# Kernel tuning notes

Measured on AMD Instinct MI355X. Metric: run time of the kernel, lower is better.

Reference implementation:

```python
import jax, jax.numpy as jnp
import numpy as np

T = 524288          # 2**19 hash table size per level (power of 2)
F = 2               # features per table entry
NL = [16, 22, 30, 42, 58, 80, 111, 153, 212, 293, 406, 561, 775, 1071, 1481, 2046]
L_DIR = 4           # direction positional encoding freqs: 3 + 2*4*3 = 27
AABB = 3.0
PI1, PI2, PI3 = 1, 2654435761, 805459861
N_PTS = 1000000

_BITS = np.array([[(v >> k) & 1 for k in range(3)] for v in range(8)], dtype=bool)  # [8,3] corner offsets


def _linear(key, fan_in, fan_out):
    lim = 1.0 / np.sqrt(fan_in)
    kw, kb = jax.random.split(key)
    W = jax.random.uniform(kw, (fan_in, fan_out), jnp.float32, -lim, lim)
    b = jax.random.uniform(kb, (fan_out,), jnp.float32, -lim, lim)
    return W, b


def setup_inputs() -> dict:
    key = jax.random.key(0)
    ks = jax.random.split(key, 8)
    x = jax.random.normal(ks[0], (N_PTS, 3), jnp.float32)   # world-space sample points
    d = jax.random.normal(ks[1], (N_PTS, 3), jnp.float32)   # view directions
    tables = (jax.random.uniform(ks[2], (len(NL), T, F), jnp.float32) * 2 - 1) * 1e-4
    dW1, db1 = _linear(ks[3], F * len(NL), 64)
    dW2, db2 = _linear(ks[4], 64, 16)
    cW1, cb1 = _linear(ks[5], 27 + 16, 64)
    cW2, cb2 = _linear(ks[6], 64, 64)
    cW3, cb3 = _linear(ks[7], 64, 3)
    return dict(x=x, d=d, tables=tables, dW1=dW1, db1=db1, dW2=dW2, db2=db2,
                cW1=cW1, cb1=cb1, cW2=cW2, cb2=cb2, cW3=cW3, cb3=cb3)


def _hash_encode(xs, tables):
    # xs: [n,3] in [0,1]^3. Multi-resolution hash grid + trilinear interpolation.
    bits = jnp.asarray(_BITS)  # [8,3] bool
    feats = []
    for i, n in enumerate(NL):
        xn = xs * n
        fl = jnp.floor(xn)
        w = xn - fl                                   # [n,3] trilinear weights
        fl_i = fl.astype(jnp.uint32)
        ce_i = jnp.ceil(xn).astype(jnp.uint32)
        corner = jnp.where(bits[None], ce_i[:, None, :], fl_i[:, None, :])   # [n,8,3]
        # spatial hash: xor of coord * prime, mod T; T is 2**19 so uint32
        # wraparound multiply is exact mod T (bit-mask)
        h = ((corner[..., 0] * jnp.uint32(PI1))
             ^ (corner[..., 1] * jnp.uint32(PI2))
             ^ (corner[..., 2] * jnp.uint32(PI3))) & jnp.uint32(T - 1)       # [n,8]
        vals = tables[i][h]                            # [n,8,F] irregular gather
        wc = jnp.prod(jnp.where(bits[None], w[:, None, :], 1.0 - w[:, None, :]), axis=-1)  # [n,8]
        feats.append(jnp.einsum('nv,nvf->nf', wc, vals))
    return jnp.concatenate(feats, axis=1)              # [n, F*len(NL)] = [n,32]


def _pos_enc(d):
    outs = [d]
    for i in range(L_DIR):
        outs.append(jnp.sin((2.0 ** i) * d))
        outs.append(jnp.cos((2.0 ** i) * d))
    return jnp.concatenate(outs, axis=1)               # [n,27]


def reference(x, d, tables, dW1, db1, dW2, db2, cW1, cb1, cW2, cb2, cW3, cb3):
    xs = x / AABB
    mask = (jnp.abs(xs[:, 0]) < 0.5) & (jnp.abs(xs[:, 1]) < 0.5) & (jnp.abs(xs[:, 2]) < 0.5)
    xs = jnp.clip(xs + 0.5, 0.0, 1.0)                  # out-of-box rows get masked below
    feats = _hash_encode(xs, tables)
    h = jnp.maximum(feats @ dW1 + db1, 0.0) @ dW2 + db2            # [n,16] density MLP
    c_in = jnp.concatenate([h, _pos_enc(d)], axis=1)               # [n,43]
    hid = jnp.maximum(c_in @ cW1 + cb1, 0.0)
    hid = jnp.maximum(hid @ cW2 + cb2, 0.0)
    col = jax.nn.sigmoid(hid @ cW3 + cb3)                          # [n,3]
    color = jnp.where(mask[:, None], col, 0.0)
    log_sigma = jnp.where(mask, h[:, 0], -10000.0)
    return color, jnp.exp(log_sigma)
```

## Files before the change

### kernel.cpp

```cpp
#include <hip/hip_runtime.h>
#include <hip/hip_bf16.h>
#include <stdint.h>

#define TS 524288u
#define TMASK (TS - 1u)
#define QTOTAL 331757
#define NHL 11

typedef __attribute__((ext_vector_type(8))) short bf16x8;
typedef __attribute__((ext_vector_type(4))) float f32x4;

__device__ __forceinline__ short f2bf(float f) {
    union { float f; uint32_t u; } v; v.f = f;
    const uint32_t r = (v.u + 0x7fffu + ((v.u >> 16) & 1u)) >> 16;
    return (short)r;
}
__device__ __forceinline__ uint32_t cvtpk(float a, float b) {
    uint32_t r;
    asm("v_cvt_pk_bf16_f32 %0, %1, %2" : "=v"(r) : "v"(a), "v"(b));
    return r;
}
__device__ __forceinline__ short bf1(float a) { return (short)(cvtpk(a, a) & 0xffffu); }
__device__ __forceinline__ float bflo(uint32_t u) { return __uint_as_float(u << 16); }
__device__ __forceinline__ float bfhi(uint32_t u) { return __uint_as_float(u & 0xffff0000u); }
__device__ __forceinline__ uint32_t pack2(float a, float b) {
    return (uint32_t)(uint16_t)f2bf(a) | ((uint32_t)(uint16_t)f2bf(b) << 16);
}

__constant__ float c_NLf[16] = {16.f,22.f,30.f,42.f,58.f,80.f,111.f,153.f,
                                212.f,293.f,406.f,561.f,775.f,1071.f,1481.f,2046.f};
__constant__ int c_NP1[5]  = {17, 23, 31, 43, 59};
__constant__ int c_QOFF[5] = {0, 4913, 17080, 46871, 126378};

__global__ __launch_bounds__(256)
void cvt_tables_h(const float2* __restrict__ src, uint32_t* __restrict__ dst, int npairs)
{
    const int i = blockIdx.x * 256 + threadIdx.x;
    if (i >= npairs) return;
    const float2 v = src[i];
    dst[i] = pack2(v.x, v.y);
}

__global__ __launch_bounds__(256)
void build_quad(const float2* __restrict__ tbf, uint4* __restrict__ quad)
{
    const int i = blockIdx.x * 256 + threadIdx.x;
    if (i >= QTOTAL) return;
    int l, base;
    if      (i <   4913) { l = 0; base = 0;      }
    else if (i <  17080) { l = 1; base = 4913;   }
    else if (i <  46871) { l = 2; base = 17080;  }
    else if (i < 126378) { l = 3; base = 46871;  }
    else                 { l = 4; base = 126378; }
    const int np1 = c_NP1[l];
    int r = i - base;
    const int z = r % np1; r /= np1;
    const int y = r % np1;
    const int x = r / np1;
    const float2* tb = tbf + (size_t)l * TS;
    const uint32_t hx  = (uint32_t)x;
    const uint32_t hy0 = (uint32_t)y       * 2654435761u;
    const uint32_t hy1 = (uint32_t)(y + 1) * 2654435761u;
    const uint32_t hz0 = (uint32_t)z       * 805459861u;
    const uint32_t hz1 = (uint32_t)(z + 1) * 805459861u;
    const float2 a = tb[(hx ^ hy0 ^ hz0) & TMASK];
    const float2 b = tb[(hx ^ hy0 ^ hz1) & TMASK];
    const float2 c = tb[(hx ^ hy1 ^ hz0) & TMASK];
    const float2 d = tb[(hx ^ hy1 ^ hz1) & TMASK];
    uint4 q;
    q.x = pack2(a.x, a.y);
    q.y = pack2(b.x, b.y);
    q.z = pack2(c.x, c.y);
    q.w = pack2(d.x, d.y);
    quad[i] = q;
}

__device__ __forceinline__ uint32_t enc_pt(const int l, const float sx, const float sy,
                                           const float sz,
                                           const uint32_t* __restrict__ tb16h,
                                           const uint4* __restrict__ qtab)
{
    const float nf = c_NLf[l];
    const float xn0 = sx * nf, xn1 = sy * nf, xn2 = sz * nf;
    const float fl0 = floorf(xn0), fl1 = floorf(xn1), fl2 = floorf(xn2);
    const float w0 = xn0 - fl0, w1 = xn1 - fl1, w2 = xn2 - fl2;
    const uint32_t f0 = (uint32_t)fl0, f1 = (uint32_t)fl1, f2 = (uint32_t)fl2;

    float v0x,v0y,v1x,v1y,v2x,v2y,v3x,v3y,v4x,v4y,v5x,v5y,v6x,v6y,v7x,v7y;

    if (l < 5) {
        const int np1 = c_NP1[l];
        const uint4* qt = qtab + c_QOFF[l];
        const int cell = ((int)f0 * np1 + (int)f1) * np1 + (int)f2;
        const uint4 qa = qt[cell];
        const uint4 qb = qt[cell + np1 * np1];
        v0x = bflo(qa.x); v0y = bfhi(qa.x);
        v4x = bflo(qa.y); v4y = bfhi(qa.y);
        v2x = bflo(qa.z); v2y = bfhi(qa.z);
        v6x = bflo(qa.w); v6y = bfhi(qa.w);
        v1x = bflo(qb.x); v1y = bfhi(qb.x);
        v5x = bflo(qb.y); v5y = bfhi(qb.y);
        v3x = bflo(qb.z); v3y = bfhi(qb.z);
        v7x = bflo(qb.w); v7y = bfhi(qb.w);
    } else {
        const uint32_t c0 = (uint32_t)ceilf(xn0);
        const uint32_t c1 = (uint32_t)ceilf(xn1);
        const uint32_t c2 = (uint32_t)ceilf(xn2);
        const uint32_t hyf = f1 * 2654435761u, hyc = c1 * 2654435761u;
        const uint32_t hzf = f2 * 805459861u,  hzc = c2 * 805459861u;
        const uint32_t* tb = tb16h + (size_t)(l - 5) * TS;
        const uint32_t Sff = hyf ^ hzf, Scf = hyc ^ hzf;
        const uint32_t Sfc = hyf ^ hzc, Scc = hyc ^ hzc;
        uint32_t e0,e1,e2,e3,e4,e5,e6,e7;
        if ((f0 ^ c0) == 1u) {
            const uint32_t h0 = (f0 ^ Sff) & TMASK;
            const uint32_t h2 = (f0 ^ Scf) & TMASK;
            const uint32_t h4 = (f0 ^ Sfc) & TMASK;
            const uint32_t h6 = (f0 ^ Scc) & TMASK;
            const uint2 t0 = *reinterpret_cast<const uint2*>(tb + (h0 & ~1u));
            const uint2 t2 = *reinterpret_cast<const uint2*>(tb + (h2 & ~1u));
            const uint2 t4 = *reinterpret_cast<const uint2*>(tb + (h4 & ~1u));
            const uint2 t6 = *reinterpret_cast<const uint2*>(tb + (h6 & ~1u));
            e0 = (h0 & 1u) ? t0.y : t0.x;  e1 = (h0 & 1u) ? t0.x : t0.y;
            e2 = (h2 & 1u) ? t2.y : t2.x;  e3 = (h2 & 1u) ? t2.x : t2.y;
            e4 = (h4 & 1u) ? t4.y : t4.x;  e5 = (h4 & 1u) ? t4.x : t4.y;
            e6 = (h6 & 1u) ? t6.y : t6.x;  e7 = (h6 & 1u) ? t6.x : t6.y;
        } else {
            e0 = tb[(f0 ^ Sff) & TMASK];  e1 = tb[(c0 ^ Sff) & TMASK];
            e2 = tb[(f0 ^ Scf) & TMASK];  e3 = tb[(c0 ^ Scf) & TMASK];
            e4 = tb[(f0 ^ Sfc) & TMASK];  e5 = tb[(c0 ^ Sfc) & TMASK];
            e6 = tb[(f0 ^ Scc) & TMASK];  e7 = tb[(c0 ^ Scc) & TMASK];
        }
        v0x = bflo(e0); v0y = bfhi(e0); v1x = bflo(e1); v1y = bfhi(e1);
        v2x = bflo(e2); v2y = bfhi(e2); v3x = bflo(e3); v3y = bfhi(e3);
        v4x = bflo(e4); v4y = bfhi(e4); v5x = bflo(e5); v5y = bfhi(e5);
        v6x = bflo(e6); v6y = bfhi(e6); v7x = bflo(e7); v7y = bfhi(e7);
    }

    const float u0 = 1.0f - w0, u1 = 1.0f - w1, u2 = 1.0f - w2;
    float a0, a1;
    a0 = u0*u1*u2 * v0x;              a1 = u0*u1*u2 * v0y;
    a0 = fmaf(w0*u1*u2, v1x, a0);     a1 = fmaf(w0*u1*u2, v1y, a1);
    a0 = fmaf(u0*w1*u2, v2x, a0);     a1 = fmaf(u0*w1*u2, v2y, a1);
    a0 = fmaf(w0*w1*u2, v3x, a0);     a1 = fmaf(w0*w1*u2, v3y, a1);
    a0 = fmaf(u0*u1*w2, v4x, a0);     a1 = fmaf(u0*u1*w2, v4y, a1);
    a0 = fmaf(w0*u1*w2, v5x, a0);     a1 = fmaf(w0*u1*w2, v5y, a1);
    a0 = fmaf(u0*w1*w2, v6x, a0);     a1 = fmaf(u0*w1*w2, v6y, a1);
    a0 = fmaf(w0*w1*w2, v7x, a0);     a1 = fmaf(w0*w1*w2, v7y, a1);

    return cvtpk(a0, a1);
}

__global__ __launch_bounds__(256)
void ngp_encode_lm(const float* __restrict__ xg, const uint32_t* __restrict__ tb16h,
                   const uint4* __restrict__ qtab, uint32_t* __restrict__ feats_lm,
                   const int n, const unsigned tiles)
{
    const unsigned b = blockIdx.x;
    const int l = (int)(b / tiles);
    const int p = (int)(b - (unsigned)l * tiles) * 256 + threadIdx.x;
    if (p >= n) return;

    float sx = xg[3*p+0] / 3.0f, sy = xg[3*p+1] / 3.0f, sz = xg[3*p+2] / 3.0f;
    if (!((fabsf(sx) < 0.5f) && (fabsf(sy) < 0.5f) && (fabsf(sz) < 0.5f))) {
        feats_lm[(size_t)l * n + p] = 0u;
        return;
    }
    sx = fminf(fmaxf(sx + 0.5f, 0.0f), 1.0f);
    sy = fminf(fmaxf(sy + 0.5f, 0.0f), 1.0f);
    sz = fminf(fmaxf(sz + 0.5f, 0.0f), 1.0f);
    feats_lm[(size_t)l * n + p] = enc_pt(l, sx, sy, sz, tb16h, qtab);
}

__global__ __launch_bounds__(256)
void ngp_encode_f32(const float* __restrict__ xg, const float2* __restrict__ tbf,
                    uint32_t* __restrict__ feats_lm, const int n, const unsigned tiles)
{
    const unsigned b = blockIdx.x;
    const int l = (int)(b / tiles);
    const int p = (int)(b - (unsigned)l * tiles) * 256 + threadIdx.x;
    if (p >= n) return;
    float sx = xg[3*p+0] / 3.0f, sy = xg[3*p+1] / 3.0f, sz = xg[3*p+2] / 3.0f;
    if (!((fabsf(sx) < 0.5f) && (fabsf(sy) < 0.5f) && (fabsf(sz) < 0.5f))) {
        feats_lm[(size_t)l * n + p] = 0u;
        return;
    }
    sx = fminf(fmaxf(sx + 0.5f, 0.0f), 1.0f);
    sy = fminf(fmaxf(sy + 0.5f, 0.0f), 1.0f);
    sz = fminf(fmaxf(sz + 0.5f, 0.0f), 1.0f);
    const float nf = c_NLf[l];
    const float xn0 = sx*nf, xn1 = sy*nf, xn2 = sz*nf;
    const float fl0 = floorf(xn0), fl1 = floorf(xn1), fl2 = floorf(xn2);
    const float w0 = xn0-fl0, w1 = xn1-fl1, w2 = xn2-fl2;
    const uint32_t f0=(uint32_t)fl0, f1=(uint32_t)fl1, f2=(uint32_t)fl2;
    const uint32_t c0=(uint32_t)ceilf(xn0), c1=(uint32_t)ceilf(xn1), c2=(uint32_t)ceilf(xn2);
    const uint32_t hyf = f1*2654435761u, hyc = c1*2654435761u;
    const uint32_t hzf = f2*805459861u,  hzc = c2*805459861u;
    const float2* tb = tbf + (size_t)l * TS;
    const float2 e0 = tb[(f0^hyf^hzf)&TMASK], e1 = tb[(c0^hyf^hzf)&TMASK];
    const float2 e2 = tb[(f0^hyc^hzf)&TMASK], e3 = tb[(c0^hyc^hzf)&TMASK];
    const float2 e4 = tb[(f0^hyf^hzc)&TMASK], e5 = tb[(c0^hyf^hzc)&TMASK];
    const float2 e6 = tb[(f0^hyc^hzc)&TMASK], e7 = tb[(c0^hyc^hzc)&TMASK];
    const float u0 = 1.0f-w0, u1 = 1.0f-w1, u2 = 1.0f-w2;
    float a0, a1;
    a0 = u0*u1*u2 * e0.x;             a1 = u0*u1*u2 * e0.y;
    a0 = fmaf(w0*u1*u2, e1.x, a0);    a1 = fmaf(w0*u1*u2, e1.y, a1);
    a0 = fmaf(u0*w1*u2, e2.x, a0);    a1 = fmaf(u0*w1*u2, e2.y, a1);
    a0 = fmaf(w0*w1*u2, e3.x, a0);    a1 = fmaf(w0*w1*u2, e3.y, a1);
    a0 = fmaf(u0*u1*w2, e4.x, a0);    a1 = fmaf(u0*u1*w2, e4.y, a1);
    a0 = fmaf(w0*u1*w2, e5.x, a0);    a1 = fmaf(w0*u1*w2, e5.y, a1);
    a0 = fmaf(u0*w1*w2, e6.x, a0);    a1 = fmaf(u0*w1*w2, e6.y, a1);
    a0 = fmaf(w0*w1*w2, e7.x, a0);    a1 = fmaf(w0*w1*w2, e7.y, a1);
    feats_lm[(size_t)l * n + p] = pack2(a0, a1);
}

#define ACT_STRIDE 72

__global__ __launch_bounds__(256, 2)
void ngp_mlp_mfma(const float* __restrict__ xg, const float* __restrict__ dg,
                  const uint32_t* __restrict__ feats_lm,
                  const float* __restrict__ dW1, const float* __restrict__ db1,
                  const float* __restrict__ dW2, const float* __restrict__ db2,
                  const float* __restrict__ cW1, const float* __restrict__ cb1,
                  const float* __restrict__ cW2, const float* __restrict__ cb2,
                  const float* __restrict__ cW3, const float* __restrict__ cb3,
                  float* __restrict__ out, int n)
{
    __shared__ __align__(16) short w1[2048];
    __shared__ __align__(16) short w2[1024];
    __shared__ __align__(16) short w3[4096];
    __shared__ __align__(16) short w4[4096];
    __shared__ __align__(16) short w5[1024];
    __shared__ __align__(16) float b1[64];
    __shared__ __align__(16) float b2[16];
    __shared__ __align__(16) float b3[64];
    __shared__ __align__(16) float b4[64];
    __shared__ __align__(16) float b5[16];
    __shared__ __align__(16) short act[4][16*ACT_STRIDE];

    const int tid = threadIdx.x;

    for (int i2 = tid; i2 < 4*16*ACT_STRIDE/2; i2 += 256)
        reinterpret_cast<uint32_t*>(act)[i2] = 0u;

    for (int i2 = tid; i2 < 2048; i2 += 256) {
        const int jb = i2 >> 9, lane = (i2 >> 3) & 63, e = i2 & 7;
        const int j = jb*16 + (lane & 15), k = ((lane >> 4) << 3) + e;
        w1[i2] = f2bf(dW1[k*64 + j]);
    }
    for (int i2 = tid; i2 < 1024; i2 += 256) {
        const int kb = i2 >> 9, lane = (i2 >> 3) & 63, e = i2 & 7;
        const int j = lane & 15, k = kb*32 + ((lane >> 4) << 3) + e;
        w2[i2] = f2bf(dW2[k*16 + j]);
    }
    for (int i2 = tid; i2 < 4096; i2 += 256) {
        const int jb = i2 >> 10, kb = (i2 >> 9) & 1, lane = (i2 >> 3) & 63, e = i2 & 7;
        const int j = jb*16 + (lane & 15), k = kb*32 + ((lane >> 4) << 3) + e;
        w3[i2] = (k < 43) ? f2bf(cW1[k*64 + j]) : (short)0;
        w4[i2] = f2bf(cW2[k*64 + j]);
    }
    for (int i2 = tid; i2 < 1024; i2 += 256) {
        const int kb = i2 >> 9, lane = (i2 >> 3) & 63, e = i2 & 7;
        const int j = lane & 15, k = kb*32 + ((lane >> 4) << 3) + e;
        w5[i2] = (j < 3) ? f2bf(cW3[k*3 + j]) : (short)0;
    }
    if (tid < 64) { b1[tid] = db1[tid]; b3[tid] = cb1[tid]; b4[tid] = cb2[tid]; }
    if (tid < 16) { b2[tid] = db2[tid]; b5[tid] = (tid < 3) ? cb3[tid] : 0.0f; }
    __syncthreads();

    const int wv = tid >> 6, lane = tid & 63;
    const int p16 = lane & 15, quad = lane >> 4;
    const int dc = (quad < 3) ? quad : 0;
    short* buf = &act[wv][0];

    bf16x8 A1[4], A2[2], A3[8], A4[8], A5[2];
    #pragma unroll
    for (int jb = 0; jb < 4; ++jb) A1[jb] = *reinterpret_cast<const bf16x8*>(&w1[(jb*64 + lane)*8]);
    #pragma unroll
    for (int kb = 0; kb < 2; ++kb) A2[kb] = *reinterpret_cast<const bf16x8*>(&w2[(kb*64 + lane)*8]);
    #pragma unroll
    for (int i = 0; i < 8; ++i) {
        A3[i] = *reinterpret_cast<const bf16x8*>(&w3[(i*64 + lane)*8]);
        A4[i] = *reinterpret_cast<const bf16x8*>(&w4[(i*64 + lane)*8]);
    }
    #pragma unroll
    for (int kb = 0; kb < 2; ++kb) A5[kb] = *reinterpret_cast<const bf16x8*>(&w5[(kb*64 + lane)*8]);
    f32x4 B1[4], B3[4], B4[4];
    #pragma unroll
    for (int jb = 0; jb < 4; ++jb) {
        B1[jb] = *reinterpret_cast<const f32x4*>(&b1[jb*16 + quad*4]);
        B3[jb] = *reinterpret_cast<const f32x4*>(&b3[jb*16 + quad*4]);
        B4[jb] = *reinterpret_cast<const f32x4*>(&b4[jb*16 + quad*4]);
    }
    const f32x4 B2v = *reinterpret_cast<const f32x4*>(&b2[quad*4]);
    const f32x4 B5v = *reinterpret_cast<const f32x4*>(&b5[quad*4]);

    const int ntiles = (n + 63) >> 6;
    int t = blockIdx.x;
    if (t >= ntiles) return;

    int pp_n; bool valid_n;
    uint32_t fn0, fn1, fn2, fn3;
    float xn0, xn1, xn2, dn;

    auto issue = [&](int tt) {
        const int pr = tt*64 + wv*16 + p16;
        valid_n = (pr < n);
        pp_n = valid_n ? pr : (n - 1);
        fn0 = feats_lm[(size_t)(4*quad+0)*n + pp_n];
        fn1 = feats_lm[(size_t)(4*quad+1)*n + pp_n];
        fn2 = feats_lm[(size_t)(4*quad+2)*n + pp_n];
        fn3 = feats_lm[(size_t)(4*quad+3)*n + pp_n];
        xn0 = xg[3*pp_n+0];
        xn1 = xg[3*pp_n+1];
        xn2 = xg[3*pp_n+2];
        dn  = dg[3*pp_n + dc];
    };

    issue(t);
    while (t < ntiles) {
        const int pp = pp_n;
        const bool valid = valid_n;
        const uint32_t fc0 = fn0, fc1 = fn1, fc2 = fn2, fc3 = fn3;
        const float xc0 = xn0, xc1 = xn1, xc2 = xn2;
        const float dv = dn;

        const int t2 = t + gridDim.x;
        if (t2 < ntiles) issue(t2);

        const bool inside = (fabsf(xc0 / 3.0f) < 0.5f) && (fabsf(xc1 / 3.0f) < 0.5f)
                         && (fabsf(xc2 / 3.0f) < 0.5f);

        union { int4 i; bf16x8 v; } bu;
        bu.i.x = (int)fc0; bu.i.y = (int)fc1; bu.i.z = (int)fc2; bu.i.w = (int)fc3;
        const bf16x8 bA = bu.v;
        #pragma unroll
        for (int jb = 0; jb < 4; ++jb) {
            const int j0 = jb*16 + quad*4;
            f32x4 acc = B1[jb];
            acc = __builtin_amdgcn_mfma_f32_16x16x32_bf16(A1[jb], bA, acc, 0, 0, 0);
            uint2 s;
            s.x = cvtpk(fmaxf(acc[0], 0.f), fmaxf(acc[1], 0.f));
            s.y = cvtpk(fmaxf(acc[2], 0.f), fmaxf(acc[3], 0.f));
            *reinterpret_cast<uint2*>(&buf[p16*ACT_STRIDE + j0]) = s;
        }

        {
            const bf16x8 bF0 = *reinterpret_cast<const bf16x8*>(&buf[p16*ACT_STRIDE + quad*8]);
            const bf16x8 bF1 = *reinterpret_cast<const bf16x8*>(&buf[p16*ACT_STRIDE + 32 + quad*8]);
            f32x4 acc2 = B2v;
            acc2 = __builtin_amdgcn_mfma_f32_16x16x32_bf16(A2[0], bF0, acc2, 0, 0, 0);
            acc2 = __builtin_amdgcn_mfma_f32_16x16x32_bf16(A2[1], bF1, acc2, 0, 0, 0);
            if (quad == 0 && valid)
                out[(size_t)3*n + pp] = inside ? __expf(acc2[0]) : 0.0f;
            uint2 s;
            s.x = cvtpk(acc2[0], acc2[1]);
            s.y = cvtpk(acc2[2], acc2[3]);
            *reinterpret_cast<uint2*>(&buf[p16*ACT_STRIDE + quad*4]) = s;
        }
        if (quad < 3) {
            buf[p16*ACT_STRIDE + 16 + quad] = bf1(dv);
            float arg = dv;
            #pragma unroll
            for (int f = 0; f < 4; ++f) {
                buf[p16*ACT_STRIDE + 19 + 6*f + quad] = bf1(__sinf(arg));
                buf[p16*ACT_STRIDE + 22 + 6*f + quad] = bf1(__cosf(arg));
                arg += arg;
            }
        }

        {
            const bf16x8 bF0 = *reinterpret_cast<const bf16x8*>(&buf[p16*ACT_STRIDE + quad*8]);
            const bf16x8 bF1 = *reinterpret_cast<const bf16x8*>(&buf[p16*ACT_STRIDE + 32 + quad*8]);
            #pragma unroll
            for (int jb = 0; jb < 4; ++jb) {
                const int j0 = jb*16 + quad*4;
                f32x4 acc = B3[jb];
                acc = __builtin_amdgcn_mfma_f32_16x16x32_bf16(A3[jb*2 + 0], bF0, acc, 0, 0, 0);
                acc = __builtin_amdgcn_mfma_f32_16x16x32_bf16(A3[jb*2 + 1], bF1, acc, 0, 0, 0);
                uint2 s;
                s.x = cvtpk(fmaxf(acc[0], 0.f), fmaxf(acc[1], 0.f));
                s.y = cvtpk(fmaxf(acc[2], 0.f), fmaxf(acc[3], 0.f));
                *reinterpret_cast<uint2*>(&buf[p16*ACT_STRIDE + j0]) = s;
            }
        }

        {
            const bf16x8 bF0 = *reinterpret_cast<const bf16x8*>(&buf[p16*ACT_STRIDE + quad*8]);
            const bf16x8 bF1 = *reinterpret_cast<const bf16x8*>(&buf[p16*ACT_STRIDE + 32 + quad*8]);
            #pragma unroll
            for (int jb = 0; jb < 4; ++jb) {
                const int j0 = jb*16 + quad*4;
                f32x4 acc = B4[jb];
                acc = __builtin_amdgcn_mfma_f32_16x16x32_bf16(A4[jb*2 + 0], bF0, acc, 0, 0, 0);
                acc = __builtin_amdgcn_mfma_f32_16x16x32_bf16(A4[jb*2 + 1], bF1, acc, 0, 0, 0);
                uint2 s;
                s.x = cvtpk(fmaxf(acc[0], 0.f), fmaxf(acc[1], 0.f));
                s.y = cvtpk(fmaxf(acc[2], 0.f), fmaxf(acc[3], 0.f));
                *reinterpret_cast<uint2*>(&buf[p16*ACT_STRIDE + j0]) = s;
            }
        }

        {
            const bf16x8 bF0 = *reinterpret_cast<const bf16x8*>(&buf[p16*ACT_STRIDE + quad*8]);
            const bf16x8 bF1 = *reinterpret_cast<const bf16x8*>(&buf[p16*ACT_STRIDE + 32 + quad*8]);
            f32x4 acc5 = B5v;
            acc5 = __builtin_amdgcn_mfma_f32_16x16x32_bf16(A5[0], bF0, acc5, 0, 0, 0);
            acc5 = __builtin_amdgcn_mfma_f32_16x16x32_bf16(A5[1], bF1, acc5, 0, 0, 0);
            if (quad == 0 && valid) {
                #pragma unroll
                for (int r = 0; r < 3; ++r) {
                    const float s = 1.0f / (1.0f + __expf(-acc5[r]));
                    out[3*(size_t)pp + r] = inside ? s : 0.0f;
                }
            }
        }
        t = t2;
    }
}

extern "C" void kernel_launch(void* const* d_in, const int* in_sizes, int n_in,
                              void* d_out, int out_size, void* d_ws, size_t ws_size,
                              hipStream_t stream)
{
    const float* x   = (const float*)d_in[0];
    const float* d   = (const float*)d_in[1];
    const float* tb  = (const float*)d_in[2];
    const float* dW1 = (const float*)d_in[3];
    const float* db1 = (const float*)d_in[4];
    const float* dW2 = (const float*)d_in[5];
    const float* db2 = (const float*)d_in[6];
    const float* cW1 = (const float*)d_in[7];
    const float* cb1 = (const float*)d_in[8];
    const float* cW2 = (const float*)d_in[9];
    const float* cb2 = (const float*)d_in[10];
    const float* cW3 = (const float*)d_in[11];
    const float* cb3 = (const float*)d_in[12];
    float* out = (float*)d_out;

    const int n = in_sizes[0] / 3;

    size_t off = 0;
    uint32_t* feats_lm = (uint32_t*)d_ws;                 off += (size_t)n * 16 * 4;
    uint32_t* tb16h    = (uint32_t*)((char*)d_ws + off);  off += (size_t)NHL * TS * 4;
    uint4*    quadbuf  = (uint4*)((char*)d_ws + off);     off += (size_t)QTOTAL * 16;
    const bool planA = (ws_size >= off);

    const unsigned tiles = (unsigned)((n + 255) / 256);

    if (planA) {
        {
            const int npairs = NHL * (int)TS;
            hipLaunchKernelGGL(cvt_tables_h, dim3((npairs + 255) / 256), dim3(256), 0, stream,
                               (const float2*)tb + 5 * (size_t)TS, tb16h, npairs);
        }
        hipLaunchKernelGGL(build_quad, dim3((QTOTAL + 255) / 256), dim3(256), 0, stream,
                           (const float2*)tb, quadbuf);
        hipLaunchKernelGGL(ngp_encode_lm, dim3(tiles * 16), dim3(256), 0, stream,
                           x, tb16h, quadbuf, feats_lm, n, tiles);
    } else {
        hipLaunchKernelGGL(ngp_encode_f32, dim3(tiles * 16), dim3(256), 0, stream,
                           x, (const float2*)tb, feats_lm, n, tiles);
    }
    {
        const int ntiles = (n + 63) >> 6;
        const int nblk = (ntiles < 512) ? ntiles : 512;
        dim3 block(256), grid(nblk);
        hipLaunchKernelGGL(ngp_mlp_mfma, grid, block, 0, stream,
                           x, d, feats_lm, dW1, db1, dW2, db2,
                           cW1, cb1, cW2, cb2, cW3, cb3, out, n);
    }
}
```

Before: 367.5 us.

## Precompute normalized points once and raise MLP occupancy with bias reloads

Adds a prep kernel that normalizes and clips the sample points once, marking out-of-box points with a sentinel, so the 16 per-level encode blocks and the MLP no longer repeat the divide and box test. The MLP kernel stops holding biases in registers and reads them from shared memory, moves launch bounds from 2 to 3 waves per SIMD, widens the grid cap from 512 to 768 blocks, and pads the activation stride from 72 to 76. The cost is an extra kernel launch plus a 12-byte-per-point buffer write and read, and the encode kernel still reads three floats per point.

```diff
diff --git a/kernel.cpp b/kernel.cpp
--- a/kernel.cpp
+++ b/kernel.cpp
@@ -73,6 +73,26 @@
     q.z = pack2(c.x, c.y);
     q.w = pack2(d.x, d.y);
     quad[i] = q;
+}
+
+__global__ __launch_bounds__(256)
+void prep_pts(const float* __restrict__ xg, float* __restrict__ prep, int n)
+{
+    const int i = blockIdx.x * 256 + threadIdx.x;
+    if (i >= n) return;
+    const float sx = xg[3*i+0] / 3.0f;
+    const float sy = xg[3*i+1] / 3.0f;
+    const float sz = xg[3*i+2] / 3.0f;
+    const bool inside = (fabsf(sx) < 0.5f) && (fabsf(sy) < 0.5f) && (fabsf(sz) < 0.5f);
+    if (inside) {
+        prep[3*i+0] = fminf(fmaxf(sx + 0.5f, 0.0f), 1.0f);
+        prep[3*i+1] = fminf(fmaxf(sy + 0.5f, 0.0f), 1.0f);
+        prep[3*i+2] = fminf(fmaxf(sz + 0.5f, 0.0f), 1.0f);
+    } else {
+        prep[3*i+0] = -1.0f;
+        prep[3*i+1] = 0.0f;
+        prep[3*i+2] = 0.0f;
+    }
 }
 
 __device__ __forceinline__ uint32_t enc_pt(const int l, const float sx, const float sy,
@@ -151,8 +171,9 @@
     return cvtpk(a0, a1);
 }
 
+template<bool HASPREP>
 __global__ __launch_bounds__(256)
-void ngp_encode_lm(const float* __restrict__ xg, const uint32_t* __restrict__ tb16h,
+void ngp_encode_lm(const float* __restrict__ xp, const uint32_t* __restrict__ tb16h,
                    const uint4* __restrict__ qtab, uint32_t* __restrict__ feats_lm,
                    const int n, const unsigned tiles)
 {
@@ -161,15 +182,21 @@
     const int p = (int)(b - (unsigned)l * tiles) * 256 + threadIdx.x;
     if (p >= n) return;
 
-    float sx = xg[3*p+0] / 3.0f, sy = xg[3*p+1] / 3.0f, sz = xg[3*p+2] / 3.0f;
-    if (!((fabsf(sx) < 0.5f) && (fabsf(sy) < 0.5f) && (fabsf(sz) < 0.5f))) {
-        feats_lm[(size_t)l * n + p] = 0u;
-        return;
-    }
-    sx = fminf(fmaxf(sx + 0.5f, 0.0f), 1.0f);
-    sy = fminf(fmaxf(sy + 0.5f, 0.0f), 1.0f);
-    sz = fminf(fmaxf(sz + 0.5f, 0.0f), 1.0f);
-    feats_lm[(size_t)l * n + p] = enc_pt(l, sx, sy, sz, tb16h, qtab);
+    if (HASPREP) {
+        const float s0 = xp[3*p+0], s1 = xp[3*p+1], s2 = xp[3*p+2];
+        if (s0 < 0.0f) { feats_lm[(size_t)l * n + p] = 0u; return; }
+        feats_lm[(size_t)l * n + p] = enc_pt(l, s0, s1, s2, tb16h, qtab);
+    } else {
+        float sx = xp[3*p+0] / 3.0f, sy = xp[3*p+1] / 3.0f, sz = xp[3*p+2] / 3.0f;
+        if (!((fabsf(sx) < 0.5f) && (fabsf(sy) < 0.5f) && (fabsf(sz) < 0.5f))) {
+            feats_lm[(size_t)l * n + p] = 0u;
+            return;
+        }
+        sx = fminf(fmaxf(sx + 0.5f, 0.0f), 1.0f);
+        sy = fminf(fmaxf(sy + 0.5f, 0.0f), 1.0f);
+        sz = fminf(fmaxf(sz + 0.5f, 0.0f), 1.0f);
+        feats_lm[(size_t)l * n + p] = enc_pt(l, sx, sy, sz, tb16h, qtab);
+    }
 }
 
 __global__ __launch_bounds__(256)
@@ -214,10 +241,11 @@
     feats_lm[(size_t)l * n + p] = pack2(a0, a1);
 }
 
-#define ACT_STRIDE 72
-
-__global__ __launch_bounds__(256, 2)
-void ngp_mlp_mfma(const float* __restrict__ xg, const float* __restrict__ dg,
+#define ACT_STRIDE 76
+
+template<bool HASPREP>
+__global__ __launch_bounds__(256, 3)
+void ngp_mlp_mfma(const float* __restrict__ xp, const float* __restrict__ dg,
                   const uint32_t* __restrict__ feats_lm,
                   const float* __restrict__ dW1, const float* __restrict__ db1,
                   const float* __restrict__ dW2, const float* __restrict__ db2,
@@ -285,15 +313,6 @@
     }
     #pragma unroll
     for (int kb = 0; kb < 2; ++kb) A5[kb] = *reinterpret_cast<const bf16x8*>(&w5[(kb*64 + lane)*8]);
-    f32x4 B1[4], B3[4], B4[4];
-    #pragma unroll
-    for (int jb = 0; jb < 4; ++jb) {
-        B1[jb] = *reinterpret_cast<const f32x4*>(&b1[jb*16 + quad*4]);
-        B3[jb] = *reinterpret_cast<const f32x4*>(&b3[jb*16 + quad*4]);
-        B4[jb] = *reinterpret_cast<const f32x4*>(&b4[jb*16 + quad*4]);
-    }
-    const f32x4 B2v = *reinterpret_cast<const f32x4*>(&b2[quad*4]);
-    const f32x4 B5v = *reinterpret_cast<const f32x4*>(&b5[quad*4]);
 
     const int ntiles = (n + 63) >> 6;
     int t = blockIdx.x;
@@ -301,7 +320,7 @@
 
     int pp_n; bool valid_n;
     uint32_t fn0, fn1, fn2, fn3;
-    float xn0, xn1, xn2, dn;
+    float in0, in1, in2, dn;
 
     auto issue = [&](int tt) {
         const int pr = tt*64 + wv*16 + p16;
@@ -311,9 +330,13 @@
         fn1 = feats_lm[(size_t)(4*quad+1)*n + pp_n];
         fn2 = feats_lm[(size_t)(4*quad+2)*n + pp_n];
         fn3 = feats_lm[(size_t)(4*quad+3)*n + pp_n];
-        xn0 = xg[3*pp_n+0];
-        xn1 = xg[3*pp_n+1];
-        xn2 = xg[3*pp_n+2];
+        if (HASPREP) {
+            in0 = xp[3*pp_n];
+        } else {
+            in0 = xp[3*pp_n+0];
+            in1 = xp[3*pp_n+1];
+            in2 = xp[3*pp_n+2];
+        }
         dn  = dg[3*pp_n + dc];
     };
 
@@ -322,14 +345,19 @@
         const int pp = pp_n;
         const bool valid = valid_n;
         const uint32_t fc0 = fn0, fc1 = fn1, fc2 = fn2, fc3 = fn3;
-        const float xc0 = xn0, xc1 = xn1, xc2 = xn2;
+        const float ic0 = in0, ic1 = in1, ic2 = in2;
         const float dv = dn;
 
         const int t2 = t + gridDim.x;
         if (t2 < ntiles) issue(t2);
 
-        const bool inside = (fabsf(xc0 / 3.0f) < 0.5f) && (fabsf(xc1 / 3.0f) < 0.5f)
-                         && (fabsf(xc2 / 3.0f) < 0.5f);
+        bool inside;
+        if (HASPREP) {
+            inside = (ic0 >= 0.0f);
+        } else {
+            inside = (fabsf(ic0 / 3.0f) < 0.5f) && (fabsf(ic1 / 3.0f) < 0.5f)
+                  && (fabsf(ic2 / 3.0f) < 0.5f);
+        }
 
         union { int4 i; bf16x8 v; } bu;
         bu.i.x = (int)fc0; bu.i.y = (int)fc1; bu.i.z = (int)fc2; bu.i.w = (int)fc3;
@@ -337,7 +365,7 @@
         #pragma unroll
         for (int jb = 0; jb < 4; ++jb) {
             const int j0 = jb*16 + quad*4;
-            f32x4 acc = B1[jb];
+            f32x4 acc = *reinterpret_cast<const f32x4*>(&b1[j0]);
             acc = __builtin_amdgcn_mfma_f32_16x16x32_bf16(A1[jb], bA, acc, 0, 0, 0);
             uint2 s;
             s.x = cvtpk(fmaxf(acc[0], 0.f), fmaxf(acc[1], 0.f));
@@ -348,7 +376,7 @@
         {
             const bf16x8 bF0 = *reinterpret_cast<const bf16x8*>(&buf[p16*ACT_STRIDE + quad*8]);
             const bf16x8 bF1 = *reinterpret_cast<const bf16x8*>(&buf[p16*ACT_STRIDE + 32 + quad*8]);
-            f32x4 acc2 = B2v;
+            f32x4 acc2 = *reinterpret_cast<const f32x4*>(&b2[quad*4]);
             acc2 = __builtin_amdgcn_mfma_f32_16x16x32_bf16(A2[0], bF0, acc2, 0, 0, 0);
             acc2 = __builtin_amdgcn_mfma_f32_16x16x32_bf16(A2[1], bF1, acc2, 0, 0, 0);
             if (quad == 0 && valid)
@@ -375,7 +403,7 @@
             #pragma unroll
             for (int jb = 0; jb < 4; ++jb) {
                 const int j0 = jb*16 + quad*4;
-                f32x4 acc = B3[jb];
+                f32x4 acc = *reinterpret_cast<const f32x4*>(&b3[j0]);
                 acc = __builtin_amdgcn_mfma_f32_16x16x32_bf16(A3[jb*2 + 0], bF0, acc, 0, 0, 0);
                 acc = __builtin_amdgcn_mfma_f32_16x16x32_bf16(A3[jb*2 + 1], bF1, acc, 0, 0, 0);
                 uint2 s;
@@ -391,7 +419,7 @@
             #pragma unroll
             for (int jb = 0; jb < 4; ++jb) {
                 const int j0 = jb*16 + quad*4;
-                f32x4 acc = B4[jb];
+                f32x4 acc = *reinterpret_cast<const f32x4*>(&b4[j0]);
                 acc = __builtin_amdgcn_mfma_f32_16x16x32_bf16(A4[jb*2 + 0], bF0, acc, 0, 0, 0);
                 acc = __builtin_amdgcn_mfma_f32_16x16x32_bf16(A4[jb*2 + 1], bF1, acc, 0, 0, 0);
                 uint2 s;
@@ -404,7 +432,7 @@
         {
             const bf16x8 bF0 = *reinterpret_cast<const bf16x8*>(&buf[p16*ACT_STRIDE + quad*8]);
             const bf16x8 bF1 = *reinterpret_cast<const bf16x8*>(&buf[p16*ACT_STRIDE + 32 + quad*8]);
-            f32x4 acc5 = B5v;
+            f32x4 acc5 = *reinterpret_cast<const f32x4*>(&b5[quad*4]);
             acc5 = __builtin_amdgcn_mfma_f32_16x16x32_bf16(A5[0], bF0, acc5, 0, 0, 0);
             acc5 = __builtin_amdgcn_mfma_f32_16x16x32_bf16(A5[1], bF1, acc5, 0, 0, 0);
             if (quad == 0 && valid) {
@@ -444,9 +472,15 @@
     uint32_t* feats_lm = (uint32_t*)d_ws;                 off += (size_t)n * 16 * 4;
     uint32_t* tb16h    = (uint32_t*)((char*)d_ws + off);  off += (size_t)NHL * TS * 4;
     uint4*    quadbuf  = (uint4*)((char*)d_ws + off);     off += (size_t)QTOTAL * 16;
-    const bool planA = (ws_size >= off);
+    const size_t off1 = off;
+    float*    prepbuf  = (float*)((char*)d_ws + off);     off += (size_t)n * 3 * 4;
+    const size_t off2 = off;
+    const bool planA  = (ws_size >= off1);
+    const bool planA2 = (ws_size >= off2);
 
     const unsigned tiles = (unsigned)((n + 255) / 256);
+    const int ntiles = (n + 63) >> 6;
+    const int nblk = (ntiles < 768) ? ntiles : 768;
 
     if (planA) {
         {
@@ -456,17 +490,25 @@
         }
         hipLaunchKernelGGL(build_quad, dim3((QTOTAL + 255) / 256), dim3(256), 0, stream,
                            (const float2*)tb, quadbuf);
-        hipLaunchKernelGGL(ngp_encode_lm, dim3(tiles * 16), dim3(256), 0, stream,
-                           x, tb16h, quadbuf, feats_lm, n, tiles);
+        if (planA2) {
+            hipLaunchKernelGGL(prep_pts, dim3((n + 255) / 256), dim3(256), 0, stream,
+                               x, prepbuf, n);
+            hipLaunchKernelGGL((ngp_encode_lm<true>), dim3(tiles * 16), dim3(256), 0, stream,
+                               prepbuf, tb16h, quadbuf, feats_lm, n, tiles);
+            hipLaunchKernelGGL((ngp_mlp_mfma<true>), dim3(nblk), dim3(256), 0, stream,
+                               prepbuf, d, feats_lm, dW1, db1, dW2, db2,
+                               cW1, cb1, cW2, cb2, cW3, cb3, out, n);
+        } else {
+            hipLaunchKernelGGL((ngp_encode_lm<false>), dim3(tiles * 16), dim3(256), 0, stream,
+                               x, tb16h, quadbuf, feats_lm, n, tiles);
+            hipLaunchKernelGGL((ngp_mlp_mfma<false>), dim3(nblk), dim3(256), 0, stream,
+                               x, d, feats_lm, dW1, db1, dW2, db2,
+                               cW1, cb1, cW2, cb2, cW3, cb3, out, n);
+        }
     } else {
         hipLaunchKernelGGL(ngp_encode_f32, dim3(tiles * 16), dim3(256), 0, stream,
                            x, (const float2*)tb, feats_lm, n, tiles);
-    }
-    {
-        const int ntiles = (n + 63) >> 6;
-        const int nblk = (ntiles < 512) ? ntiles : 512;
-        dim3 block(256), grid(nblk);
-        hipLaunchKernelGGL(ngp_mlp_mfma, grid, block, 0, stream,
+        hipLaunchKernelGGL((ngp_mlp_mfma<false>), dim3(nblk), dim3(256), 0, stream,
                            x, d, feats_lm, dW1, db1, dW2, db2,
                            cW1, cb1, cW2, cb2, cW3, cb3, out, n);
     }
```

Result: slower. 406.8 us (+10.7%).

## Process two 16-point tiles per wave in MLP kernel and use nontemporal feature stores

Applied to the files above, without the earlier changes.

The MLP kernel now interleaves two independent 16-point sub-tiles per wave (A and B), each with its own LDS activation buffer, so back-to-back MFMAs on independent data can hide MFMA and LDS latency. Biases are now read from LDS at each use instead of being held in registers, which frees VGPRs for the doubled state. The encode kernel writes features with nontemporal stores, so these streaming writes are less likely to evict hash-table lines from cache. Risks are higher register pressure and doubled LDS use per block, which could lower occupancy, and fewer persistent tiles per block.

```diff
diff --git a/kernel.cpp b/kernel.cpp
--- a/kernel.cpp
+++ b/kernel.cpp
@@ -163,13 +163,14 @@
 
     float sx = xg[3*p+0] / 3.0f, sy = xg[3*p+1] / 3.0f, sz = xg[3*p+2] / 3.0f;
     if (!((fabsf(sx) < 0.5f) && (fabsf(sy) < 0.5f) && (fabsf(sz) < 0.5f))) {
-        feats_lm[(size_t)l * n + p] = 0u;
+        __builtin_nontemporal_store(0u, &feats_lm[(size_t)l * n + p]);
         return;
     }
     sx = fminf(fmaxf(sx + 0.5f, 0.0f), 1.0f);
     sy = fminf(fmaxf(sy + 0.5f, 0.0f), 1.0f);
     sz = fminf(fmaxf(sz + 0.5f, 0.0f), 1.0f);
-    feats_lm[(size_t)l * n + p] = enc_pt(l, sx, sy, sz, tb16h, qtab);
+    const uint32_t fv = enc_pt(l, sx, sy, sz, tb16h, qtab);
+    __builtin_nontemporal_store(fv, &feats_lm[(size_t)l * n + p]);
 }
 
 __global__ __launch_bounds__(256)
@@ -236,11 +237,11 @@
     __shared__ __align__(16) float b3[64];
     __shared__ __align__(16) float b4[64];
     __shared__ __align__(16) float b5[16];
-    __shared__ __align__(16) short act[4][16*ACT_STRIDE];
+    __shared__ __align__(16) short act[4][32*ACT_STRIDE];
 
     const int tid = threadIdx.x;
 
-    for (int i2 = tid; i2 < 4*16*ACT_STRIDE/2; i2 += 256)
+    for (int i2 = tid; i2 < 4*32*ACT_STRIDE/2; i2 += 256)
         reinterpret_cast<uint32_t*>(act)[i2] = 0u;
 
     for (int i2 = tid; i2 < 2048; i2 += 256) {
@@ -271,7 +272,8 @@
     const int wv = tid >> 6, lane = tid & 63;
     const int p16 = lane & 15, quad = lane >> 4;
     const int dc = (quad < 3) ? quad : 0;
-    short* buf = &act[wv][0];
+    short* bufA = &act[wv][0];
+    short* bufB = &act[wv][16*ACT_STRIDE];
 
     bf16x8 A1[4], A2[2], A3[8], A4[8], A5[2];
     #pragma unroll
@@ -285,133 +287,169 @@
     }
     #pragma unroll
     for (int kb = 0; kb < 2; ++kb) A5[kb] = *reinterpret_cast<const bf16x8*>(&w5[(kb*64 + lane)*8]);
-    f32x4 B1[4], B3[4], B4[4];
-    #pragma unroll
-    for (int jb = 0; jb < 4; ++jb) {
-        B1[jb] = *reinterpret_cast<const f32x4*>(&b1[jb*16 + quad*4]);
-        B3[jb] = *reinterpret_cast<const f32x4*>(&b3[jb*16 + quad*4]);
-        B4[jb] = *reinterpret_cast<const f32x4*>(&b4[jb*16 + quad*4]);
-    }
-    const f32x4 B2v = *reinterpret_cast<const f32x4*>(&b2[quad*4]);
-    const f32x4 B5v = *reinterpret_cast<const f32x4*>(&b5[quad*4]);
-
-    const int ntiles = (n + 63) >> 6;
+
+    const int ntiles = (n + 127) >> 7;
     int t = blockIdx.x;
     if (t >= ntiles) return;
 
-    int pp_n; bool valid_n;
-    uint32_t fn0, fn1, fn2, fn3;
-    float xn0, xn1, xn2, dn;
+    int ppA_n, ppB_n; bool vA_n, vB_n;
+    uint32_t fA0,fA1,fA2,fA3, fB0,fB1,fB2,fB3;
+    float xA0,xA1,xA2, xB0,xB1,xB2, dA_n, dB_n;
 
     auto issue = [&](int tt) {
-        const int pr = tt*64 + wv*16 + p16;
-        valid_n = (pr < n);
-        pp_n = valid_n ? pr : (n - 1);
-        fn0 = feats_lm[(size_t)(4*quad+0)*n + pp_n];
-        fn1 = feats_lm[(size_t)(4*quad+1)*n + pp_n];
-        fn2 = feats_lm[(size_t)(4*quad+2)*n + pp_n];
-        fn3 = feats_lm[(size_t)(4*quad+3)*n + pp_n];
-        xn0 = xg[3*pp_n+0];
-        xn1 = xg[3*pp_n+1];
-        xn2 = xg[3*pp_n+2];
-        dn  = dg[3*pp_n + dc];
+        const int prA = tt*128 + wv*16 + p16;
+        const int prB = prA + 64;
+        vA_n = (prA < n);  ppA_n = vA_n ? prA : (n - 1);
+        vB_n = (prB < n);  ppB_n = vB_n ? prB : (n - 1);
+        fA0 = feats_lm[(size_t)(4*quad+0)*n + ppA_n];
+        fA1 = feats_lm[(size_t)(4*quad+1)*n + ppA_n];
+        fA2 = feats_lm[(size_t)(4*quad+2)*n + ppA_n];
+        fA3 = feats_lm[(size_t)(4*quad+3)*n + ppA_n];
+        fB0 = feats_lm[(size_t)(4*quad+0)*n + ppB_n];
+        fB1 = feats_lm[(size_t)(4*quad+1)*n + ppB_n];
+        fB2 = feats_lm[(size_t)(4*quad+2)*n + ppB_n];
+        fB3 = feats_lm[(size_t)(4*quad+3)*n + ppB_n];
+        xA0 = xg[3*ppA_n+0]; xA1 = xg[3*ppA_n+1]; xA2 = xg[3*ppA_n+2];
+        xB0 = xg[3*ppB_n+0]; xB1 = xg[3*ppB_n+1]; xB2 = xg[3*ppB_n+2];
+        dA_n = dg[3*ppA_n + dc];
+        dB_n = dg[3*ppB_n + dc];
     };
 
     issue(t);
     while (t < ntiles) {
-        const int pp = pp_n;
-        const bool valid = valid_n;
-        const uint32_t fc0 = fn0, fc1 = fn1, fc2 = fn2, fc3 = fn3;
-        const float xc0 = xn0, xc1 = xn1, xc2 = xn2;
-        const float dv = dn;
+        const int ppA = ppA_n, ppB = ppB_n;
+        const bool vA = vA_n, vB = vB_n;
+        const uint32_t a0 = fA0, a1 = fA1, a2 = fA2, a3 = fA3;
+        const uint32_t b0 = fB0, b1v = fB1, b2v = fB2, b3v = fB3;
+        const float cA0 = xA0, cA1 = xA1, cA2 = xA2;
+        const float cB0 = xB0, cB1 = xB1, cB2 = xB2;
+        const float dvA = dA_n, dvB = dB_n;
 
         const int t2 = t + gridDim.x;
         if (t2 < ntiles) issue(t2);
 
-        const bool inside = (fabsf(xc0 / 3.0f) < 0.5f) && (fabsf(xc1 / 3.0f) < 0.5f)
-                         && (fabsf(xc2 / 3.0f) < 0.5f);
-
-        union { int4 i; bf16x8 v; } bu;
-        bu.i.x = (int)fc0; bu.i.y = (int)fc1; bu.i.z = (int)fc2; bu.i.w = (int)fc3;
-        const bf16x8 bA = bu.v;
+        const bool inA = (fabsf(cA0/3.0f) < 0.5f) && (fabsf(cA1/3.0f) < 0.5f) && (fabsf(cA2/3.0f) < 0.5f);
+        const bool inB = (fabsf(cB0/3.0f) < 0.5f) && (fabsf(cB1/3.0f) < 0.5f) && (fabsf(cB2/3.0f) < 0.5f);
+
+        union { int4 i; bf16x8 v; } buA, buB;
+        buA.i.x = (int)a0; buA.i.y = (int)a1; buA.i.z = (int)a2; buA.i.w = (int)a3;
+        buB.i.x = (int)b0; buB.i.y = (int)b1v; buB.i.z = (int)b2v; buB.i.w = (int)b3v;
+        const bf16x8 bAa = buA.v, bAb = buB.v;
         #pragma unroll
         for (int jb = 0; jb < 4; ++jb) {
             const int j0 = jb*16 + quad*4;
-            f32x4 acc = B1[jb];
-            acc = __builtin_amdgcn_mfma_f32_16x16x32_bf16(A1[jb], bA, acc, 0, 0, 0);
-            uint2 s;
-            s.x = cvtpk(fmaxf(acc[0], 0.f), fmaxf(acc[1], 0.f));
-            s.y = cvtpk(fmaxf(acc[2], 0.f), fmaxf(acc[3], 0.f));
-            *reinterpret_cast<uint2*>(&buf[p16*ACT_STRIDE + j0]) = s;
+            const f32x4 bias = *reinterpret_cast<const f32x4*>(&b1[j0]);
+            f32x4 accA = __builtin_amdgcn_mfma_f32_16x16x32_bf16(A1[jb], bAa, bias, 0, 0, 0);
+            f32x4 accB = __builtin_amdgcn_mfma_f32_16x16x32_bf16(A1[jb], bAb, bias, 0, 0, 0);
+            uint2 sA, sB;
+            sA.x = cvtpk(fmaxf(accA[0],0.f), fmaxf(accA[1],0.f));
+            sA.y = cvtpk(fmaxf(accA[2],0.f), fmaxf(accA[3],0.f));
+            sB.x = cvtpk(fmaxf(accB[0],0.f), fmaxf(accB[1],0.f));
+            sB.y = cvtpk(fmaxf(accB[2],0.f), fmaxf(accB[3],0.f));
+            *reinterpret_cast<uint2*>(&bufA[p16*ACT_STRIDE + j0]) = sA;
+            *reinterpret_cast<uint2*>(&bufB[p16*ACT_STRIDE + j0]) = sB;
         }
 
         {
-            const bf16x8 bF0 = *reinterpret_cast<const bf16x8*>(&buf[p16*ACT_STRIDE + quad*8]);
-            const bf16x8 bF1 = *reinterpret_cast<const bf16x8*>(&buf[p16*ACT_STRIDE + 32 + quad*8]);
-            f32x4 acc2 = B2v;
-            acc2 = __builtin_amdgcn_mfma_f32_16x16x32_bf16(A2[0], bF0, acc2, 0, 0, 0);
-            acc2 = __builtin_amdgcn_mfma_f32_16x16x32_bf16(A2[1], bF1, acc2, 0, 0, 0);
-            if (quad == 0 && valid)
-                out[(size_t)3*n + pp] = inside ? __expf(acc2[0]) : 0.0f;
-            uint2 s;
-            s.x = cvtpk(acc2[0], acc2[1]);
-            s.y = cvtpk(acc2[2], acc2[3]);
-            *reinterpret_cast<uint2*>(&buf[p16*ACT_STRIDE + quad*4]) = s;
+            const bf16x8 fA0v = *reinterpret_cast<const bf16x8*>(&bufA[p16*ACT_STRIDE + quad*8]);
+            const bf16x8 fA1v = *reinterpret_cast<const bf16x8*>(&bufA[p16*ACT_STRIDE + 32 + quad*8]);
+            const bf16x8 fB0v = *reinterpret_cast<const bf16x8*>(&bufB[p16*ACT_STRIDE + quad*8]);
+            const bf16x8 fB1v = *reinterpret_cast<const bf16x8*>(&bufB[p16*ACT_STRIDE + 32 + quad*8]);
+            const f32x4 bias = *reinterpret_cast<const f32x4*>(&b2[quad*4]);
+            f32x4 accA = __builtin_amdgcn_mfma_f32_16x16x32_bf16(A2[0], fA0v, bias, 0, 0, 0);
+            f32x4 accB = __builtin_amdgcn_mfma_f32_16x16x32_bf16(A2[0], fB0v, bias, 0, 0, 0);
+            accA = __builtin_amdgcn_mfma_f32_16x16x32_bf16(A2[1], fA1v, accA, 0, 0, 0);
+            accB = __builtin_amdgcn_mfma_f32_16x16x32_bf16(A2[1], fB1v, accB, 0, 0, 0);
+            if (quad == 0 && vA) out[(size_t)3*n + ppA] = inA ? __expf(accA[0]) : 0.0f;
+            if (quad == 0 && vB) out[(size_t)3*n + ppB] = inB ? __expf(accB[0]) : 0.0f;
+            uint2 sA, sB;
+            sA.x = cvtpk(accA[0], accA[1]); sA.y = cvtpk(accA[2], accA[3]);
+            sB.x = cvtpk(accB[0], accB[1]); sB.y = cvtpk(accB[2], accB[3]);
+            *reinterpret_cast<uint2*>(&bufA[p16*ACT_STRIDE + quad*4]) = sA;
+            *reinterpret_cast<uint2*>(&bufB[p16*ACT_STRIDE + quad*4]) = sB;
         }
         if (quad < 3) {
-            buf[p16*ACT_STRIDE + 16 + quad] = bf1(dv);
-            float arg = dv;
+            bufA[p16*ACT_STRIDE + 16 + quad] = bf1(dvA);
+            bufB[p16*ACT_STRIDE + 16 + quad] = bf1(dvB);
+            float argA = dvA, argB = dvB;
             #pragma unroll
             for (int f = 0; f < 4; ++f) {
-                buf[p16*ACT_STRIDE + 19 + 6*f + quad] = bf1(__sinf(arg));
-                buf[p16*ACT_STRIDE + 22 + 6*f + quad] = bf1(__cosf(arg));
-                arg += arg;
+                bufA[p16*ACT_STRIDE + 19 + 6*f + quad] = bf1(__sinf(argA));
+                bufA[p16*ACT_STRIDE + 22 + 6*f + quad] = bf1(__cosf(argA));
+                bufB[p16*ACT_STRIDE + 19 + 6*f + quad] = bf1(__sinf(argB));
+                bufB[p16*ACT_STRIDE + 22 + 6*f + quad] = bf1(__cosf(argB));
+                argA += argA; argB += argB;
             }
         }
 
         {
-            const bf16x8 bF0 = *reinterpret_cast<const bf16x8*>(&buf[p16*ACT_STRIDE + quad*8]);
-            const bf16x8 bF1 = *reinterpret_cast<const bf16x8*>(&buf[p16*ACT_STRIDE + 32 + quad*8]);
+            const bf16x8 fA0v = *reinterpret_cast<const bf16x8*>(&bufA[p16*ACT_STRIDE + quad*8]);
+            const bf16x8 fA1v = *reinterpret_cast<const bf16x8*>(&bufA[p16*ACT_STRIDE + 32 + quad*8]);
+            const bf16x8 fB0v = *reinterpret_cast<const bf16x8*>(&bufB[p16*ACT_STRIDE + quad*8]);
+            const bf16x8 fB1v = *reinterpret_cast<const bf16x8*>(&bufB[p16*ACT_STRIDE + 32 + quad*8]);
             #pragma unroll
             for (int jb = 0; jb < 4; ++jb) {
                 const int j0 = jb*16 + quad*4;
-                f32x4 acc = B3[jb];
-                acc = __builtin_amdgcn_mfma_f32_16x16x32_bf16(A3[jb*2 + 0], bF0, acc, 0, 0, 0);
-                acc = __builtin_amdgcn_mfma_f32_16x16x32_bf16(A3[jb*2 + 1], bF1, acc, 0, 0, 0);
-                uint2 s;
-                s.x = cvtpk(fmaxf(acc[0], 0.f), fmaxf(acc[1], 0.f));
-                s.y = cvtpk(fmaxf(acc[2], 0.f), fmaxf(acc[3], 0.f));
-                *reinterpret_cast<uint2*>(&buf[p16*ACT_STRIDE + j0]) = s;
+                const f32x4 bias = *reinterpret_cast<const f32x4*>(&b3[j0]);
+                f32x4 accA = __builtin_amdgcn_mfma_f32_16x16x32_bf16(A3[jb*2+0], fA0v, bias, 0, 0, 0);
+                f32x4 accB = __builtin_amdgcn_mfma_f32_16x16x32_bf16(A3[jb*2+0], fB0v, bias, 0, 0, 0);
+                accA = __builtin_amdgcn_mfma_f32_16x16x32_bf16(A3[jb*2+1], fA1v, accA, 0, 0, 0);
+                accB = __builtin_amdgcn_mfma_f32_16x16x32_bf16(A3[jb*2+1], fB1v, accB, 0, 0, 0);
+                uint2 sA, sB;
+                sA.x = cvtpk(fmaxf(accA[0],0.f), fmaxf(accA[1],0.f));
+                sA.y = cvtpk(fmaxf(accA[2],0.f), fmaxf(accA[3],0.f));
+                sB.x = cvtpk(fmaxf(accB[0],0.f), fmaxf(accB[1],0.f));
+                sB.y = cvtpk(fmaxf(accB[2],0.f), fmaxf(accB[3],0.f));
+                *reinterpret_cast<uint2*>(&bufA[p16*ACT_STRIDE + j0]) = sA;
+                *reinterpret_cast<uint2*>(&bufB[p16*ACT_STRIDE + j0]) = sB;
             }
         }
 
         {
-            const bf16x8 bF0 = *reinterpret_cast<const bf16x8*>(&buf[p16*ACT_STRIDE + quad*8]);
-            const bf16x8 bF1 = *reinterpret_cast<const bf16x8*>(&buf[p16*ACT_STRIDE + 32 + quad*8]);
+            const bf16x8 fA0v = *reinterpret_cast<const bf16x8*>(&bufA[p16*ACT_STRIDE + quad*8]);
+            const bf16x8 fA1v = *reinterpret_cast<const bf16x8*>(&bufA[p16*ACT_STRIDE + 32 + quad*8]);
+            const bf16x8 fB0v = *reinterpret_cast<const bf16x8*>(&bufB[p16*ACT_STRIDE + quad*8]);
+            const bf16x8 fB1v = *reinterpret_cast<const bf16x8*>(&bufB[p16*ACT_STRIDE + 32 + quad*8]);
             #pragma unroll
             for (int jb = 0; jb < 4; ++jb) {
                 const int j0 = jb*16 + quad*4;
-                f32x4 acc = B4[jb];
-                acc = __builtin_amdgcn_mfma_f32_16x16x32_bf16(A4[jb*2 + 0], bF0, acc, 0, 0, 0);
-                acc = __builtin_amdgcn_mfma_f32_16x16x32_bf16(A4[jb*2 + 1], bF1, acc, 0, 0, 0);
-                uint2 s;
-                s.x = cvtpk(fmaxf(acc[0], 0.f), fmaxf(acc[1], 0.f));
-                s.y = cvtpk(fmaxf(acc[2], 0.f), fmaxf(acc[3], 0.f));
-                *reinterpret_cast<uint2*>(&buf[p16*ACT_STRIDE + j0]) = s;
+                const f32x4 bias = *reinterpret_cast<const f32x4*>(&b4[j0]);
+                f32x4 accA = __builtin_amdgcn_mfma_f32_16x16x32_bf16(A4[jb*2+0], fA0v, bias, 0, 0, 0);
+                f32x4 accB = __builtin_amdgcn_mfma_f32_16x16x32_bf16(A4[jb*2+0], fB0v, bias, 0, 0, 0);
+                accA = __builtin_amdgcn_mfma_f32_16x16x32_bf16(A4[jb*2+1], fA1v, accA, 0, 0, 0);
+                accB = __builtin_amdgcn_mfma_f32_16x16x32_bf16(A4[jb*2+1], fB1v, accB, 0, 0, 0);
+                uint2 sA, sB;
+                sA.x = cvtpk(fmaxf(accA[0],0.f), fmaxf(accA[1],0.f));
+                sA.y = cvtpk(fmaxf(accA[2],0.f), fmaxf(accA[3],0.f));
+                sB.x = cvtpk(fmaxf(accB[0],0.f), fmaxf(accB[1],0.f));
+                sB.y = cvtpk(fmaxf(accB[2],0.f), fmaxf(accB[3],0.f));
+                *reinterpret_cast<uint2*>(&bufA[p16*ACT_STRIDE + j0]) = sA;
+                *reinterpret_cast<uint2*>(&bufB[p16*ACT_STRIDE + j0]) = sB;
             }
         }
 
         {
-            const bf16x8 bF0 = *reinterpret_cast<const bf16x8*>(&buf[p16*ACT_STRIDE + quad*8]);
-            const bf16x8 bF1 = *reinterpret_cast<const bf16x8*>(&buf[p16*ACT_STRIDE + 32 + quad*8]);
-            f32x4 acc5 = B5v;
-            acc5 = __builtin_amdgcn_mfma_f32_16x16x32_bf16(A5[0], bF0, acc5, 0, 0, 0);
-            acc5 = __builtin_amdgcn_mfma_f32_16x16x32_bf16(A5[1], bF1, acc5, 0, 0, 0);
-            if (quad == 0 && valid) {
+            const bf16x8 fA0v = *reinterpret_cast<const bf16x8*>(&bufA[p16*ACT_STRIDE + quad*8]);
+            const bf16x8 fA1v = *reinterpret_cast<const bf16x8*>(&bufA[p16*ACT_STRIDE + 32 + quad*8]);
+            const bf16x8 fB0v = *reinterpret_cast<const bf16x8*>(&bufB[p16*ACT_STRIDE + quad*8]);
+            const bf16x8 fB1v = *reinterpret_cast<const bf16x8*>(&bufB[p16*ACT_STRIDE + 32 + quad*8]);
+            const f32x4 bias = *reinterpret_cast<const f32x4*>(&b5[quad*4]);
+            f32x4 accA = __builtin_amdgcn_mfma_f32_16x16x32_bf16(A5[0], fA0v, bias, 0, 0, 0);
+            f32x4 accB = __builtin_amdgcn_mfma_f32_16x16x32_bf16(A5[0], fB0v, bias, 0, 0, 0);
+            accA = __builtin_amdgcn_mfma_f32_16x16x32_bf16(A5[1], fA1v, accA, 0, 0, 0);
+            accB = __builtin_amdgcn_mfma_f32_16x16x32_bf16(A5[1], fB1v, accB, 0, 0, 0);
+            if (quad == 0 && vA) {
                 #pragma unroll
                 for (int r = 0; r < 3; ++r) {
-                    const float s = 1.0f / (1.0f + __expf(-acc5[r]));
-                    out[3*(size_t)pp + r] = inside ? s : 0.0f;
+                    const float s = 1.0f / (1.0f + __expf(-accA[r]));
+                    out[3*(size_t)ppA + r] = inA ? s : 0.0f;
+                }
+            }
+            if (quad == 0 && vB) {
+                #pragma unroll
+                for (int r = 0; r < 3; ++r) {
+                    const float s = 1.0f / (1.0f + __expf(-accB[r]));
+                    out[3*(size_t)ppB + r] = inB ? s : 0.0f;
                 }
             }
         }
@@ -447,6 +485,8 @@
     const bool planA = (ws_size >= off);
 
     const unsigned tiles = (unsigned)((n + 255) / 256);
+    const int ntiles = (n + 127) >> 7;
+    const int nblk = (ntiles < 512) ? ntiles : 512;
 
     if (planA) {
         {
@@ -462,12 +502,7 @@
         hipLaunchKernelGGL(ngp_encode_f32, dim3(tiles * 16), dim3(256), 0, stream,
                            x, (const float2*)tb, feats_lm, n, tiles);
     }
-    {
-        const int ntiles = (n + 63) >> 6;
-        const int nblk = (ntiles < 512) ? ntiles : 512;
-        dim3 block(256), grid(nblk);
-        hipLaunchKernelGGL(ngp_mlp_mfma, grid, block, 0, stream,
-                           x, d, feats_lm, dW1, db1, dW2, db2,
-                           cW1, cb1, cW2, cb2, cW3, cb3, out, n);
-    }
-}
+    hipLaunchKernelGGL(ngp_mlp_mfma, dim3(nblk), dim3(256), 0, stream,
+                       x, d, feats_lm, dW1, db1, dW2, db2,
+                       cW1, cb1, cW2, cb2, cW3, cb3, out, n);
+}
```

Measured after the change: 366.4 us. Within noise of the previous version (-0.3%).
